# Kernel optimization log

Measured on AMD Instinct MI355X. Metric: run time of the kernel, lower is better.

Reference implementation:

```python
import jax, jax.numpy as jnp
import numpy as np

GAMMA = 0.999   # from TDLoss.__init__ default
LAMBDA = 0.95   # from compute_gae default lambda_
B, S = 8192, 2048


def setup_inputs() -> dict:
    key = jax.random.key(0)
    k1, k2, k3, k4 = jax.random.split(key, 4)
    rewards = jax.random.normal(k1, (B, S), dtype=jnp.float32)
    values = jax.random.normal(k2, (B, S), dtype=jnp.float32)
    dones = jax.random.randint(k3, (B, S), 0, 2).astype(jnp.int32)
    # prefix validity mask: valid_len[b] = mask[b].sum(), as assumed by compute_gae
    lengths = jax.random.randint(k4, (B,), S // 2, S + 1)
    mask = (jnp.arange(S)[None, :] < lengths[:, None]).astype(jnp.int32)
    return {"rewards": rewards, "values": values, "dones": dones, "mask": mask}


def _gae(rewards, values, dones_f, mask, gamma, lam):
    # rewards/values/dones_f: [B,S] float; mask: [B,S] int prefix mask
    b, s = rewards.shape
    valid_len = mask.sum(axis=1)                      # [B]
    t_idx = jnp.arange(s)
    valid = t_idx[None, :] < valid_len[:, None]       # [B,S] bool
    is_last = t_idx[None, :] == (valid_len[:, None] - 1)
    # next_value = values[:, t+1], except 0 at the last valid step (and at t=S-1)
    next_vals = jnp.concatenate([values[:, 1:], jnp.zeros((b, 1), values.dtype)], axis=1)
    next_vals = jnp.where(is_last, jnp.zeros((), values.dtype), next_vals)
    nd = 1.0 - dones_f                                # (1 - done)
    delta = rewards + gamma * next_vals * nd - values

    def step(gae, xs):
        d_t, nd_t, valid_t = xs                        # each [B]
        g = d_t + gamma * lam * nd_t * gae
        g = jnp.where(valid_t, g, jnp.zeros((), d_t.dtype))  # zero outside valid prefix; resets carry
        return g, g

    xs = (delta.T, nd.T, valid.T)                     # time-major [S,B]
    _, adv_t = jax.lax.scan(step, jnp.zeros(b, rewards.dtype), xs, reverse=True)
    advantages = adv_t.T                              # [B,S]
    returns = jnp.where(valid, advantages + values, jnp.zeros((), values.dtype))
    return advantages, returns


def reference(rewards, values, dones, mask):
    return _gae(rewards, values, dones.astype(jnp.float32), mask, GAMMA, LAMBDA)
```

## Files before the change

### kernel.cpp

```cpp
#include <hip/hip_runtime.h>


static constexpr int BATCH = 8192;
static constexpr int SEQ   = 2048;
static constexpr int TBLK  = 256;
static constexpr int NBLK  = SEQ / TBLK;
static constexpr float GAMMA  = 0.999f;
static constexpr float LAMBDA = 0.95f;
static constexpr float GL     = GAMMA * LAMBDA;

__global__ __launch_bounds__(256, 4) void gae_kernel(
    const float* __restrict__ rewards,
    const float* __restrict__ values,
    const int*   __restrict__ dones,
    const int*   __restrict__ mask,
    float*       __restrict__ out)
{
    const int lane = threadIdx.x & 63;
    const int row  = blockIdx.x * 4 + (threadIdx.x >> 6);
    const size_t rowbase = (size_t)row * SEQ;

    float C    = 0.0f;
    float edge = 0.0f;

    for (int j = NBLK - 1; j >= 0; --j) {
        const size_t off = rowbase + (size_t)j * TBLK + (size_t)lane * 4;

        const float4 r4 = *reinterpret_cast<const float4*>(rewards + off);
        const float4 v4 = *reinterpret_cast<const float4*>(values  + off);
        const int4   d4 = *reinterpret_cast<const int4*>(dones + off);
        const int4   m4 = *reinterpret_cast<const int4*>(mask  + off);

        const float rr[4] = {r4.x, r4.y, r4.z, r4.w};
        const float vv[4] = {v4.x, v4.y, v4.z, v4.w};
        const int   dd[4] = {d4.x, d4.y, d4.z, d4.w};
        const int   mm[4] = {m4.x, m4.y, m4.z, m4.w};

        float a[4], b[4], vm[4];
        float mr[4], mnd[4];
        #pragma unroll
        for (int e = 0; e < 4; ++e) {
            const bool m  = (mm[e] != 0);
            const bool mn = m && (dd[e] == 0);
            vm[e]  = m ? vv[e] : 0.0f;
            mr[e]  = m ? rr[e] : 0.0f;
            mnd[e] = mn ? 1.0f : 0.0f;
            a[e]   = mn ? GL : 0.0f;
        }
        float nv3 = __shfl_down(vm[0], 1, 64);
        if (lane == 63) nv3 = edge;
        const float nv[4] = {vm[1], vm[2], vm[3], nv3};
        #pragma unroll
        for (int e = 0; e < 4; ++e)
            b[e] = mr[e] + GAMMA * nv[e] * mnd[e] - vm[e];

        float A = a[3], B = b[3];
        #pragma unroll
        for (int e = 2; e >= 0; --e) {
            B = fmaf(a[e], B, b[e]);
            A = a[e] * A;
        }

        float As = A, Bs = B;
        #pragma unroll
        for (int d = 1; d < 64; d <<= 1) {
            const float Ao = __shfl_down(As, d, 64);
            const float Bo = __shfl_down(Bs, d, 64);
            if (lane + d < 64) {
                Bs = fmaf(As, Bo, Bs);
                As = As * Ao;
            }
        }
        const float A0 = __shfl(As, 0, 64);
        const float B0 = __shfl(Bs, 0, 64);
        float cA = __shfl_down(As, 1, 64);
        float cB = __shfl_down(Bs, 1, 64);
        if (lane == 63) { cA = 1.0f; cB = 0.0f; }
        float g = fmaf(cA, C, cB);

        float adv[4], ret[4];
        #pragma unroll
        for (int e = 3; e >= 0; --e) {
            g = fmaf(a[e], g, b[e]);
            adv[e] = g;
            ret[e] = g + vm[e];
        }

        C    = fmaf(A0, C, B0);
        edge = __shfl(vm[0], 0, 64);

        *reinterpret_cast<float4*>(out + off) =
            make_float4(adv[0], adv[1], adv[2], adv[3]);
        *reinterpret_cast<float4*>(out + (size_t)BATCH * SEQ + off) =
            make_float4(ret[0], ret[1], ret[2], ret[3]);
    }
}

extern "C" void kernel_launch(void* const* d_in, const int* in_sizes, int n_in,
                              void* d_out, int out_size, void* d_ws, size_t ws_size,
                              hipStream_t stream) {
    const float* rewards = (const float*)d_in[0];
    const float* values  = (const float*)d_in[1];
    const int*   dones   = (const int*)d_in[2];
    const int*   mask    = (const int*)d_in[3];
    float* out = (float*)d_out;

    dim3 grid(BATCH / 4), block(256);
    gae_kernel<<<grid, block, 0, stream>>>(rewards, values, dones, mask, out);
}
```

Baseline: 320.3 us.

## Map one row per block and scan across waves through shared memory

Each block now handles one full row: each of 256 threads holds 8 contiguous elements, and the row is split across 4 waves. This replaces the serial loop in which one wave walked a row in 8 chunks. Per-wave scan results are combined through shared memory with two __syncthreads, so all loads for a row can be in flight at once instead of being serialized by the loop-carried dependency. The grid grows fourfold and each thread holds more registers, adding block-level barrier overhead.

```diff
diff --git a/kernel.cpp b/kernel.cpp
--- a/kernel.cpp
+++ b/kernel.cpp
@@ -3,8 +3,7 @@
 
 static constexpr int BATCH = 8192;
 static constexpr int SEQ   = 2048;
-static constexpr int TBLK  = 256;
-static constexpr int NBLK  = SEQ / TBLK;
+static constexpr int EPL   = 8;
 static constexpr float GAMMA  = 0.999f;
 static constexpr float LAMBDA = 0.95f;
 static constexpr float GL     = GAMMA * LAMBDA;
@@ -16,84 +15,100 @@
     const int*   __restrict__ mask,
     float*       __restrict__ out)
 {
+    __shared__ float sA[4], sB[4], sF[4];
+
     const int lane = threadIdx.x & 63;
-    const int row  = blockIdx.x * 4 + (threadIdx.x >> 6);
-    const size_t rowbase = (size_t)row * SEQ;
+    const int wave = threadIdx.x >> 6;
+    const int row  = blockIdx.x;
+    const size_t off = (size_t)row * SEQ + (size_t)threadIdx.x * EPL;
 
-    float C    = 0.0f;
-    float edge = 0.0f;
+    float rr[EPL], vv[EPL];
+    int   dd[EPL], mm[EPL];
+    {
+        const float4 r0 = *reinterpret_cast<const float4*>(rewards + off);
+        const float4 r1 = *reinterpret_cast<const float4*>(rewards + off + 4);
+        const float4 v0 = *reinterpret_cast<const float4*>(values  + off);
+        const float4 v1 = *reinterpret_cast<const float4*>(values  + off + 4);
+        const int4   d0 = *reinterpret_cast<const int4*>(dones + off);
+        const int4   d1 = *reinterpret_cast<const int4*>(dones + off + 4);
+        const int4   m0 = *reinterpret_cast<const int4*>(mask  + off);
+        const int4   m1 = *reinterpret_cast<const int4*>(mask  + off + 4);
+        rr[0]=r0.x; rr[1]=r0.y; rr[2]=r0.z; rr[3]=r0.w;
+        rr[4]=r1.x; rr[5]=r1.y; rr[6]=r1.z; rr[7]=r1.w;
+        vv[0]=v0.x; vv[1]=v0.y; vv[2]=v0.z; vv[3]=v0.w;
+        vv[4]=v1.x; vv[5]=v1.y; vv[6]=v1.z; vv[7]=v1.w;
+        dd[0]=d0.x; dd[1]=d0.y; dd[2]=d0.z; dd[3]=d0.w;
+        dd[4]=d1.x; dd[5]=d1.y; dd[6]=d1.z; dd[7]=d1.w;
+        mm[0]=m0.x; mm[1]=m0.y; mm[2]=m0.z; mm[3]=m0.w;
+        mm[4]=m1.x; mm[5]=m1.y; mm[6]=m1.z; mm[7]=m1.w;
+    }
 
-    for (int j = NBLK - 1; j >= 0; --j) {
-        const size_t off = rowbase + (size_t)j * TBLK + (size_t)lane * 4;
+    float a[EPL], b[EPL], vm[EPL], mr[EPL], mnd[EPL];
+    #pragma unroll
+    for (int e = 0; e < EPL; ++e) {
+        const bool m  = (mm[e] != 0);
+        const bool mn = m && (dd[e] == 0);
+        vm[e]  = m ? vv[e] : 0.0f;
+        mr[e]  = m ? rr[e] : 0.0f;
+        mnd[e] = mn ? 1.0f : 0.0f;
+        a[e]   = mn ? GL : 0.0f;
+    }
 
-        const float4 r4 = *reinterpret_cast<const float4*>(rewards + off);
-        const float4 v4 = *reinterpret_cast<const float4*>(values  + off);
-        const int4   d4 = *reinterpret_cast<const int4*>(dones + off);
-        const int4   m4 = *reinterpret_cast<const int4*>(mask  + off);
+    if (lane == 0) sF[wave] = vm[0];
+    __syncthreads();
 
-        const float rr[4] = {r4.x, r4.y, r4.z, r4.w};
-        const float vv[4] = {v4.x, v4.y, v4.z, v4.w};
-        const int   dd[4] = {d4.x, d4.y, d4.z, d4.w};
-        const int   mm[4] = {m4.x, m4.y, m4.z, m4.w};
+    float nv7 = __shfl_down(vm[0], 1, 64);
+    if (lane == 63) nv7 = (wave < 3) ? sF[wave + 1] : 0.0f;
 
-        float a[4], b[4], vm[4];
-        float mr[4], mnd[4];
-        #pragma unroll
-        for (int e = 0; e < 4; ++e) {
-            const bool m  = (mm[e] != 0);
-            const bool mn = m && (dd[e] == 0);
-            vm[e]  = m ? vv[e] : 0.0f;
-            mr[e]  = m ? rr[e] : 0.0f;
-            mnd[e] = mn ? 1.0f : 0.0f;
-            a[e]   = mn ? GL : 0.0f;
+    #pragma unroll
+    for (int e = 0; e < EPL; ++e) {
+        const float nv = (e < EPL - 1) ? vm[e + 1] : nv7;
+        b[e] = mr[e] + GAMMA * nv * mnd[e] - vm[e];
+    }
+
+    float A = a[EPL - 1], B = b[EPL - 1];
+    #pragma unroll
+    for (int e = EPL - 2; e >= 0; --e) {
+        B = fmaf(a[e], B, b[e]);
+        A = a[e] * A;
+    }
+
+    float As = A, Bs = B;
+    #pragma unroll
+    for (int d = 1; d < 64; d <<= 1) {
+        const float Ao = __shfl_down(As, d, 64);
+        const float Bo = __shfl_down(Bs, d, 64);
+        if (lane + d < 64) {
+            Bs = fmaf(As, Bo, Bs);
+            As = As * Ao;
         }
-        float nv3 = __shfl_down(vm[0], 1, 64);
-        if (lane == 63) nv3 = edge;
-        const float nv[4] = {vm[1], vm[2], vm[3], nv3};
-        #pragma unroll
-        for (int e = 0; e < 4; ++e)
-            b[e] = mr[e] + GAMMA * nv[e] * mnd[e] - vm[e];
+    }
 
-        float A = a[3], B = b[3];
-        #pragma unroll
-        for (int e = 2; e >= 0; --e) {
-            B = fmaf(a[e], B, b[e]);
-            A = a[e] * A;
-        }
+    if (lane == 0) { sA[wave] = As; sB[wave] = Bs; }
+    __syncthreads();
+    float C = 0.0f;
+    for (int w2 = 3; w2 > wave; --w2)
+        C = fmaf(sA[w2], C, sB[w2]);
 
-        float As = A, Bs = B;
-        #pragma unroll
-        for (int d = 1; d < 64; d <<= 1) {
-            const float Ao = __shfl_down(As, d, 64);
-            const float Bo = __shfl_down(Bs, d, 64);
-            if (lane + d < 64) {
-                Bs = fmaf(As, Bo, Bs);
-                As = As * Ao;
-            }
-        }
-        const float A0 = __shfl(As, 0, 64);
-        const float B0 = __shfl(Bs, 0, 64);
-        float cA = __shfl_down(As, 1, 64);
-        float cB = __shfl_down(Bs, 1, 64);
-        if (lane == 63) { cA = 1.0f; cB = 0.0f; }
-        float g = fmaf(cA, C, cB);
+    float cA = __shfl_down(As, 1, 64);
+    float cB = __shfl_down(Bs, 1, 64);
+    if (lane == 63) { cA = 1.0f; cB = 0.0f; }
+    float g = fmaf(cA, C, cB);
 
-        float adv[4], ret[4];
-        #pragma unroll
-        for (int e = 3; e >= 0; --e) {
-            g = fmaf(a[e], g, b[e]);
-            adv[e] = g;
-            ret[e] = g + vm[e];
-        }
+    float adv[EPL], ret[EPL];
+    #pragma unroll
+    for (int e = EPL - 1; e >= 0; --e) {
+        g = fmaf(a[e], g, b[e]);
+        adv[e] = g;
+        ret[e] = g + vm[e];
+    }
 
-        C    = fmaf(A0, C, B0);
-        edge = __shfl(vm[0], 0, 64);
-
-        *reinterpret_cast<float4*>(out + off) =
-            make_float4(adv[0], adv[1], adv[2], adv[3]);
-        *reinterpret_cast<float4*>(out + (size_t)BATCH * SEQ + off) =
-            make_float4(ret[0], ret[1], ret[2], ret[3]);
-    }
+    float* ap = out + off;
+    float* tp = out + (size_t)BATCH * SEQ + off;
+    *reinterpret_cast<float4*>(ap)     = make_float4(adv[0], adv[1], adv[2], adv[3]);
+    *reinterpret_cast<float4*>(ap + 4) = make_float4(adv[4], adv[5], adv[6], adv[7]);
+    *reinterpret_cast<float4*>(tp)     = make_float4(ret[0], ret[1], ret[2], ret[3]);
+    *reinterpret_cast<float4*>(tp + 4) = make_float4(ret[4], ret[5], ret[6], ret[7]);
 }
 
 extern "C" void kernel_launch(void* const* d_in, const int* in_sizes, int n_in,
@@ -105,6 +120,6 @@
     const int*   mask    = (const int*)d_in[3];
     float* out = (float*)d_out;
 
-    dim3 grid(BATCH / 4), block(256);
+    dim3 grid(BATCH), block(256);
     gae_kernel<<<grid, block, 0, stream>>>(rewards, values, dones, mask, out);
 }
```

After: 322.7 us. No clear change (+0.8%).
